# Performance work log

Hardware: AMD Instinct MI355X
Metric: run time of the kernel (lower is better)

## Reference

```python
import jax, jax.numpy as jnp
import numpy as np

B, N, D = 4, 160, 64
ZI, ZE, L, LE = 64, 64, 4, 8
H1, H2 = 128, 64


def setup_inputs() -> dict:
    key = jax.random.key(0)
    ks = jax.random.split(key, 20)
    s = 0.05
    inp = {
        "node_embeddings": jax.random.normal(ks[0], (B, N, D), jnp.float32),
        "z_intra_t": jax.random.normal(ks[1], (B, ZI), jnp.float32),
        "z_inter_t": jax.random.normal(ks[2], (B, ZE), jnp.float32),
        # lag embedding table
        "lag_emb": jax.random.normal(ks[3], (L, LE), jnp.float32),
        # instantaneous reasoner: (2D+ZI)->128->64->1
        "Wi1": jax.random.normal(ks[4], (2 * D + ZI, H1), jnp.float32) * s,
        "bi1": jnp.zeros((H1,), jnp.float32),
        "Wi2": jax.random.normal(ks[5], (H1, H2), jnp.float32) * s,
        "bi2": jnp.zeros((H2,), jnp.float32),
        "Wi3": jax.random.normal(ks[6], (H2, 1), jnp.float32) * s,
        "bi3": jnp.zeros((1,), jnp.float32),
        # lagged reasoner: (2D+ZE+LE)->128->64->1
        "Wl1": jax.random.normal(ks[7], (2 * D + ZE + LE, H1), jnp.float32) * s,
        "bl1": jnp.zeros((H1,), jnp.float32),
        "Wl2": jax.random.normal(ks[8], (H1, H2), jnp.float32) * s,
        "bl2": jnp.zeros((H2,), jnp.float32),
        "Wl3": jax.random.normal(ks[9], (H2, 1), jnp.float32) * s,
        "bl3": jnp.zeros((1,), jnp.float32),
    }
    return inp


def reference(node_embeddings, z_intra_t, z_inter_t, lag_emb,
              Wi1, bi1, Wi2, bi2, Wi3, bi3,
              Wl1, bl1, Wl2, bl2, Wl3, bl3):
    # Instead of materializing concat([h_i, h_j, z, ...]) over N*N pairs,
    # split the first linear layer's weight along its input rows; the sum of
    # per-part projections equals the linear over the concatenation.
    ne = node_embeddings  # [B, N, D]

    # --- instantaneous reasoner ---
    Wi1_a, Wi1_b, Wi1_z = Wi1[:D], Wi1[D:2 * D], Wi1[2 * D:]
    pi = ne @ Wi1_a          # [B, N, H1] projection of h_i
    pj = ne @ Wi1_b          # [B, N, H1] projection of h_j
    pz = z_intra_t @ Wi1_z   # [B, H1]
    h = jax.nn.relu(pi[:, :, None, :] + pj[:, None, :, :]
                    + pz[:, None, None, :] + bi1)          # [B, N, N, H1]
    h = jax.nn.relu(h @ Wi2 + bi2)                         # [B, N, N, H2]
    W_logits = (h @ Wi3 + bi3)[..., 0]                     # [B, N, N]

    # --- lagged reasoner ---
    Wl1_a, Wl1_b = Wl1[:D], Wl1[D:2 * D]
    Wl1_z, Wl1_l = Wl1[2 * D:2 * D + ZE], Wl1[2 * D + ZE:]
    qi = ne @ Wl1_a          # [B, N, H1]
    qj = ne @ Wl1_b          # [B, N, H1]
    qz = z_inter_t @ Wl1_z   # [B, H1]
    ql = lag_emb @ Wl1_l     # [L, H1]
    g = jax.nn.relu(qi[:, None, :, None, :] + qj[:, None, None, :, :]
                    + qz[:, None, None, None, :] + ql[None, :, None, None, :]
                    + bl1)                                 # [B, L, N, N, H1]
    g = jax.nn.relu(g @ Wl2 + bl2)                         # [B, L, N, N, H2]
    A_logits = (g @ Wl3 + bl3)[..., 0]                     # [B, L, N, N]

    mask = 1.0 - jnp.eye(N, dtype=ne.dtype)
    W_t = jax.nn.sigmoid(W_logits) * mask
    A_lags_t = jax.nn.sigmoid(A_logits) * mask
    return (W_t, A_lags_t)
```

## Files before the change

### kernel.cpp

```cpp
#include <hip/hip_runtime.h>
#include <hip/hip_bf16.h>

#define B_   4
#define N_   160
#define D_   64
#define ZI_  64
#define H1_  128
#define H2_  64
#define L_   4
#define LE_  8

typedef __bf16 bf16x8 __attribute__((ext_vector_type(8)));
typedef float  f32x4  __attribute__((ext_vector_type(4)));

__global__ __launch_bounds__(128) void stage_a(
    const float* __restrict__ ne,
    const float* __restrict__ zi,
    const float* __restrict__ ze,
    const float* __restrict__ lag,
    const float* __restrict__ Wi1,
    const float* __restrict__ bi1,
    const float* __restrict__ Wl1,
    const float* __restrict__ bl1,
    const float* __restrict__ Wi2,
    const float* __restrict__ Wl2,
    float* __restrict__ ui, float* __restrict__ uq,
    __bf16* __restrict__ vpi, __bf16* __restrict__ vpl,
    __bf16* __restrict__ W2fi, __bf16* __restrict__ W2fl)
{
    const int bi = blockIdx.x;
    const int b  = bi / N_;
    const int h  = threadIdx.x;

    const float* nerow = ne + bi * D_;

    float pi_ = 0.f, pj_ = 0.f, qi_ = 0.f, qj_ = 0.f;
#pragma unroll 16
    for (int d = 0; d < D_; ++d) {
        const float a = nerow[d];
        pi_ += a * Wi1[d * H1_ + h];
        pj_ += a * Wi1[(D_ + d) * H1_ + h];
        qi_ += a * Wl1[d * H1_ + h];
        qj_ += a * Wl1[(D_ + d) * H1_ + h];
    }
    float pz = 0.f, qz = 0.f;
#pragma unroll 16
    for (int z = 0; z < ZI_; ++z) {
        pz += zi[b * ZI_ + z] * Wi1[(2 * D_ + z) * H1_ + h];
        qz += ze[b * ZI_ + z] * Wl1[(2 * D_ + z) * H1_ + h];
    }

    ui[bi * H1_ + h]  = pi_ + pz + bi1[h];
    vpi[bi * H1_ + h] = (__bf16)pj_;
    vpl[bi * H1_ + h] = (__bf16)qj_;

    const float qbase = qi_ + qz + bl1[h];
#pragma unroll
    for (int l = 0; l < L_; ++l) {
        float ql = 0.f;
#pragma unroll
        for (int e = 0; e < LE_; ++e)
            ql += lag[l * LE_ + e] * Wl1[(2 * D_ + ZI_ + e) * H1_ + h];
        uq[((b * L_ + l) * N_ + (bi % N_)) * H1_ + h] = qbase + ql;
    }

    if (bi < 2) {
        const float* Wsrc = (bi == 0) ? Wi2 : Wl2;
        __bf16* Wdst = (bi == 0) ? W2fi : W2fl;
#pragma unroll
        for (int r = 0; r < 8; ++r) {
            const int fc = h + 128 * r;
            const int kt = fc >> 8, ct = (fc >> 6) & 3;
            const int q = (fc >> 4) & 3, c = fc & 15;
            bf16x8 t;
#pragma unroll
            for (int j = 0; j < 8; ++j)
                t[j] = (__bf16)Wsrc[(32 * kt + 8 * q + j) * H2_ + 16 * ct + c];
            *(bf16x8*)(Wdst + fc * 8) = t;
        }
    }
}

__global__ __launch_bounds__(256, 2) void stage_b(
    const float* __restrict__ ui, const float* __restrict__ uq,
    const __bf16* __restrict__ vpi, const __bf16* __restrict__ vpl,
    const __bf16* __restrict__ W2fi, const __bf16* __restrict__ W2fl,
    const float* __restrict__ bi2, const float* __restrict__ bi3,
    const float* __restrict__ bl2, const float* __restrict__ bl3,
    const float* __restrict__ Wi3, const float* __restrict__ Wl3,
    float* __restrict__ out)
{
    __shared__ __bf16 panel[N_ * H1_];

    const int t    = threadIdx.x;
    const int wid  = t >> 6;
    const int lane = t & 63;
    const int q = lane >> 4;
    const int c = lane & 15;

    const int blk  = blockIdx.x;
    const int wave = blk * 4 + wid;

    const __bf16 *psrc, *Wf;
    if (blk < 160) { psrc = vpi + (blk / 40) * (N_ * H1_);          Wf = W2fi; }
    else           { psrc = vpl + ((blk - 160) / 160) * (N_ * H1_); Wf = W2fl; }

    const float* ubase;
    const float *b2, *w3;
    float b3f;
    long  obase;
    int   i;
    if (wave < B_ * N_) {
        i = wave % N_;
        ubase = ui + wave * H1_;
        b2 = bi2; w3 = Wi3; b3f = bi3[0];
        obase = (long)wave * N_;
    } else {
        const int w2i = wave - B_ * N_;
        i = w2i % N_;
        ubase = uq + w2i * H1_;
        b2 = bl2; w3 = Wl3; b3f = bl3[0];
        obase = (long)B_ * N_ * N_ + (long)w2i * N_;
    }

    bf16x8 stg[10];
#pragma unroll
    for (int it = 0; it < 10; ++it)
        stg[it] = *(const bf16x8*)(psrc + 2048 * it + 8 * t);

    bf16x8 bfr[4][4];
#pragma unroll
    for (int kt = 0; kt < 4; ++kt)
#pragma unroll
        for (int ct = 0; ct < 4; ++ct)
            bfr[kt][ct] = *(const bf16x8*)(Wf + ((kt * 4 + ct) * 64 + lane) * 8);

    f32x4 u0[4], u1[4];
#pragma unroll
    for (int kt = 0; kt < 4; ++kt) {
        const float* up = ubase + 32 * kt + 8 * q;
        u0[kt] = *(const f32x4*)(up);
        u1[kt] = *(const f32x4*)(up + 4);
    }

    float b2c[4], w3c[4];
#pragma unroll
    for (int ct = 0; ct < 4; ++ct) {
        b2c[ct] = b2[16 * ct + c];
        w3c[ct] = w3[16 * ct + c];
    }

    {
        const int gsw = (t & 15) ^ ((t >> 4) & 7);
        const int rowbase = (t >> 4) * H1_ + gsw * 8;
#pragma unroll
        for (int it = 0; it < 10; ++it)
            *(bf16x8*)(panel + 16 * it * H1_ + rowbase) = stg[it];
    }
    __syncthreads();

    for (int jt = 0; jt < 10; ++jt) {
        const __bf16* prow = panel + (16 * jt + c) * H1_;
        f32x4 acc[4];
#pragma unroll
        for (int ct = 0; ct < 4; ++ct)
            acc[ct] = (f32x4){b2c[ct], b2c[ct], b2c[ct], b2c[ct]};

#pragma unroll
        for (int kt = 0; kt < 4; ++kt) {
            const bf16x8 vb = *(const bf16x8*)(prow + (((4 * kt + q) ^ (c & 7)) << 3));
            bf16x8 a;
#pragma unroll
            for (int j = 0; j < 4; ++j) {
                a[j]     = (__bf16)fmaxf(u0[kt][j] + (float)vb[j],     0.f);
                a[4 + j] = (__bf16)fmaxf(u1[kt][j] + (float)vb[4 + j], 0.f);
            }
#pragma unroll
            for (int ct = 0; ct < 4; ++ct)
                acc[ct] = __builtin_amdgcn_mfma_f32_16x16x32_bf16(
                    a, bfr[kt][ct], acc[ct], 0, 0, 0);
        }

        float logit[4];
#pragma unroll
        for (int r = 0; r < 4; ++r) {
            float p = 0.f;
#pragma unroll
            for (int ct = 0; ct < 4; ++ct) {
                const float h2 = fmaxf(acc[ct][r], 0.f);
                p += h2 * w3c[ct];
            }
            p += __shfl_xor(p, 1);
            p += __shfl_xor(p, 2);
            p += __shfl_xor(p, 4);
            p += __shfl_xor(p, 8);
            logit[r] = p;
        }

        if (c < 4) {
            const int j = 16 * jt + 4 * q + c;
            const float lg = logit[c] + b3f;
            const float s = (j == i) ? 0.f : 1.f / (1.f + __expf(-lg));
            out[obase + j] = s;
        }
    }
}

extern "C" void kernel_launch(void* const* d_in, const int* in_sizes, int n_in,
                              void* d_out, int out_size, void* d_ws, size_t ws_size,
                              hipStream_t stream) {
    const float* ne  = (const float*)d_in[0];
    const float* zi  = (const float*)d_in[1];
    const float* ze  = (const float*)d_in[2];
    const float* lag = (const float*)d_in[3];
    const float* Wi1 = (const float*)d_in[4];
    const float* bi1 = (const float*)d_in[5];
    const float* Wi2 = (const float*)d_in[6];
    const float* bi2 = (const float*)d_in[7];
    const float* Wi3 = (const float*)d_in[8];
    const float* bi3 = (const float*)d_in[9];
    const float* Wl1 = (const float*)d_in[10];
    const float* bl1 = (const float*)d_in[11];
    const float* Wl2 = (const float*)d_in[12];
    const float* bl2 = (const float*)d_in[13];
    const float* Wl3 = (const float*)d_in[14];
    const float* bl3 = (const float*)d_in[15];

    float*  ws   = (float*)d_ws;
    float*  ui   = ws;
    float*  uqw  = ws + 81920;
    __bf16* vpi  = (__bf16*)(ws + 409600);
    __bf16* vpl  = vpi + 81920;
    __bf16* W2fi = (__bf16*)(ws + 491520);
    __bf16* W2fl = W2fi + 8192;

    stage_a<<<B_ * N_, 128, 0, stream>>>(ne, zi, ze, lag, Wi1, bi1, Wl1, bl1,
                                         Wi2, Wl2, ui, uqw, vpi, vpl, W2fi, W2fl);

    stage_b<<<(B_ * N_ + B_ * L_ * N_) / 4, 256, 0, stream>>>(
        ui, uqw, vpi, vpl, W2fi, W2fl,
        bi2, bi3, bl2, bl3, Wi3, Wl3,
        (float*)d_out);
}
```

Before: 113.8 us.

## Split stage_b column range across two blocks and batch logit reductions

Each stage_b block now handles half of the j columns (80 rows of the panel), doubling the grid to 1600 blocks and halving LDS per block. This is meant to raise parallelism and occupancy and shorten each block's critical path. The jt loop is also fully unrolled, with the cross-lane shuffle reductions and sigmoid stores deferred until after all MFMA work so they can be batched. In exchange, u/W2 fragment loads and the block prologue are duplicated across twice as many blocks, and register pressure rises.

```diff
diff --git a/kernel.cpp b/kernel.cpp
--- a/kernel.cpp
+++ b/kernel.cpp
@@ -90,7 +90,7 @@
     const float* __restrict__ Wi3, const float* __restrict__ Wl3,
     float* __restrict__ out)
 {
-    __shared__ __bf16 panel[N_ * H1_];
+    __shared__ __bf16 panel[80 * H1_];
 
     const int t    = threadIdx.x;
     const int wid  = t >> 6;
@@ -98,34 +98,38 @@
     const int q = lane >> 4;
     const int c = lane & 15;
 
-    const int blk  = blockIdx.x;
-    const int wave = blk * 4 + wid;
+    const int blk    = blockIdx.x;
+    const int rowgrp = blk >> 1;
+    const int half   = blk & 1;
+    const int wave   = rowgrp * 4 + wid;
 
     const __bf16 *psrc, *Wf;
-    if (blk < 160) { psrc = vpi + (blk / 40) * (N_ * H1_);          Wf = W2fi; }
-    else           { psrc = vpl + ((blk - 160) / 160) * (N_ * H1_); Wf = W2fl; }
+    if (rowgrp < 160) { psrc = vpi + (rowgrp / 40) * (N_ * H1_);           Wf = W2fi; }
+    else              { psrc = vpl + ((rowgrp - 160) / 160) * (N_ * H1_);  Wf = W2fl; }
+    psrc += 80 * half * H1_;
 
     const float* ubase;
     const float *b2, *w3;
-    float b3f;
+    const float* b3p;
     long  obase;
     int   i;
     if (wave < B_ * N_) {
         i = wave % N_;
         ubase = ui + wave * H1_;
-        b2 = bi2; w3 = Wi3; b3f = bi3[0];
+        b2 = bi2; w3 = Wi3; b3p = bi3;
         obase = (long)wave * N_;
     } else {
         const int w2i = wave - B_ * N_;
         i = w2i % N_;
         ubase = uq + w2i * H1_;
-        b2 = bl2; w3 = Wl3; b3f = bl3[0];
+        b2 = bl2; w3 = Wl3; b3p = bl3;
         obase = (long)B_ * N_ * N_ + (long)w2i * N_;
     }
-
-    bf16x8 stg[10];
-#pragma unroll
-    for (int it = 0; it < 10; ++it)
+    const float b3f = b3p[0];
+
+    bf16x8 stg[5];
+#pragma unroll
+    for (int it = 0; it < 5; ++it)
         stg[it] = *(const bf16x8*)(psrc + 2048 * it + 8 * t);
 
     bf16x8 bfr[4][4];
@@ -154,13 +158,15 @@
         const int gsw = (t & 15) ^ ((t >> 4) & 7);
         const int rowbase = (t >> 4) * H1_ + gsw * 8;
 #pragma unroll
-        for (int it = 0; it < 10; ++it)
+        for (int it = 0; it < 5; ++it)
             *(bf16x8*)(panel + 16 * it * H1_ + rowbase) = stg[it];
     }
     __syncthreads();
 
-    for (int jt = 0; jt < 10; ++jt) {
-        const __bf16* prow = panel + (16 * jt + c) * H1_;
+    float plog[5][4];
+#pragma unroll
+    for (int jtl = 0; jtl < 5; ++jtl) {
+        const __bf16* prow = panel + (16 * jtl + c) * H1_;
         f32x4 acc[4];
 #pragma unroll
         for (int ct = 0; ct < 4; ++ct)
@@ -181,25 +187,37 @@
                     a, bfr[kt][ct], acc[ct], 0, 0, 0);
         }
 
-        float logit[4];
 #pragma unroll
         for (int r = 0; r < 4; ++r) {
             float p = 0.f;
 #pragma unroll
-            for (int ct = 0; ct < 4; ++ct) {
-                const float h2 = fmaxf(acc[ct][r], 0.f);
-                p += h2 * w3c[ct];
-            }
+            for (int ct = 0; ct < 4; ++ct)
+                p += fmaxf(acc[ct][r], 0.f) * w3c[ct];
+            plog[jtl][r] = p;
+        }
+    }
+
+#pragma unroll
+    for (int jtl = 0; jtl < 5; ++jtl)
+#pragma unroll
+        for (int r = 0; r < 4; ++r) {
+            float p = plog[jtl][r];
             p += __shfl_xor(p, 1);
             p += __shfl_xor(p, 2);
             p += __shfl_xor(p, 4);
             p += __shfl_xor(p, 8);
-            logit[r] = p;
-        }
-
-        if (c < 4) {
-            const int j = 16 * jt + 4 * q + c;
-            const float lg = logit[c] + b3f;
+            plog[jtl][r] = p;
+        }
+
+    if (c < 4) {
+#pragma unroll
+        for (int jtl = 0; jtl < 5; ++jtl) {
+            float lg = plog[jtl][0];
+            lg = (c == 1) ? plog[jtl][1] : lg;
+            lg = (c == 2) ? plog[jtl][2] : lg;
+            lg = (c == 3) ? plog[jtl][3] : lg;
+            lg += b3f;
+            const int j = 80 * half + 16 * jtl + 4 * q + c;
             const float s = (j == i) ? 0.f : 1.f / (1.f + __expf(-lg));
             out[obase + j] = s;
         }
@@ -237,7 +255,7 @@
     stage_a<<<B_ * N_, 128, 0, stream>>>(ne, zi, ze, lag, Wi1, bi1, Wl1, bl1,
                                          Wi2, Wl2, ui, uqw, vpi, vpl, W2fi, W2fl);
 
-    stage_b<<<(B_ * N_ + B_ * L_ * N_) / 4, 256, 0, stream>>>(
+    stage_b<<<2 * (B_ * N_ + B_ * L_ * N_) / 4, 256, 0, stream>>>(
         ui, uqw, vpi, vpl, W2fi, W2fl,
         bi2, bi3, bl2, bl3, Wi3, Wl3,
         (float*)d_out);
```

Measured after the change: 117.7 us. +3.4%, slower.

## Load panel directly to LDS, pre-swizzle in stage_a, packed bf16 activation math

Applied to the files above, without the earlier changes.

Stage_a now writes the bf16 j-projection rows in the XOR-swizzled layout that stage_b reads. That lets stage_b copy the panel straight from global into LDS with global_load_lds and drop the register staging buffer. The inner loop unpacks bf16 pairs with shifts and masks, runs add and ReLU as vector ops on even/odd lanes, and repacks with a paired bf16 convert. The launch bound occupancy hint goes from 2 to 4 blocks, trading register budget for occupancy, though the 40 KB LDS panel per block may still cap residency.

```diff
diff --git a/kernel.cpp b/kernel.cpp
--- a/kernel.cpp
+++ b/kernel.cpp
@@ -12,6 +12,14 @@
 
 typedef __bf16 bf16x8 __attribute__((ext_vector_type(8)));
 typedef float  f32x4  __attribute__((ext_vector_type(4)));
+typedef unsigned int u32x4 __attribute__((ext_vector_type(4)));
+
+static __device__ __forceinline__ unsigned pk_bf16(float a, float b) {
+    __hip_bfloat162 h = __float22bfloat162_rn(float2{a, b});
+    union { __hip_bfloat162 h; unsigned u; } c;
+    c.h = h;
+    return c.u;
+}
 
 __global__ __launch_bounds__(128) void stage_a(
     const float* __restrict__ ne,
@@ -50,9 +58,11 @@
         qz += ze[b * ZI_ + z] * Wl1[(2 * D_ + z) * H1_ + h];
     }
 
-    ui[bi * H1_ + h]  = pi_ + pz + bi1[h];
-    vpi[bi * H1_ + h] = (__bf16)pj_;
-    vpl[bi * H1_ + h] = (__bf16)qj_;
+    ui[bi * H1_ + h] = pi_ + pz + bi1[h];
+
+    const int hsw = (((h >> 3) ^ (bi & 7)) << 3) | (h & 7);
+    vpi[bi * H1_ + hsw] = (__bf16)pj_;
+    vpl[bi * H1_ + hsw] = (__bf16)qj_;
 
     const float qbase = qi_ + qz + bl1[h];
 #pragma unroll
@@ -81,7 +91,7 @@
     }
 }
 
-__global__ __launch_bounds__(256, 2) void stage_b(
+__global__ __launch_bounds__(256, 4) void stage_b(
     const float* __restrict__ ui, const float* __restrict__ uq,
     const __bf16* __restrict__ vpi, const __bf16* __restrict__ vpl,
     const __bf16* __restrict__ W2fi, const __bf16* __restrict__ W2fl,
@@ -90,7 +100,7 @@
     const float* __restrict__ Wi3, const float* __restrict__ Wl3,
     float* __restrict__ out)
 {
-    __shared__ __bf16 panel[N_ * H1_];
+    __shared__ __align__(16) __bf16 panel[N_ * H1_];
 
     const int t    = threadIdx.x;
     const int wid  = t >> 6;
@@ -105,28 +115,36 @@
     if (blk < 160) { psrc = vpi + (blk / 40) * (N_ * H1_);          Wf = W2fi; }
     else           { psrc = vpl + ((blk - 160) / 160) * (N_ * H1_); Wf = W2fl; }
 
+    {
+        const char* gp = (const char*)psrc;
+        char* lp = (char*)panel;
+#pragma unroll
+        for (int it = 0; it < 10; ++it) {
+            __builtin_amdgcn_global_load_lds(
+                (const __attribute__((address_space(1))) void*)(gp + it * 4096 + t * 16),
+                (__attribute__((address_space(3))) void*)(lp + it * 4096 + wid * 1024),
+                16, 0, 0);
+        }
+    }
+
     const float* ubase;
     const float *b2, *w3;
-    float b3f;
+    const float* b3p;
     long  obase;
     int   i;
     if (wave < B_ * N_) {
         i = wave % N_;
         ubase = ui + wave * H1_;
-        b2 = bi2; w3 = Wi3; b3f = bi3[0];
+        b2 = bi2; w3 = Wi3; b3p = bi3;
         obase = (long)wave * N_;
     } else {
         const int w2i = wave - B_ * N_;
         i = w2i % N_;
         ubase = uq + w2i * H1_;
-        b2 = bl2; w3 = Wl3; b3f = bl3[0];
+        b2 = bl2; w3 = Wl3; b3p = bl3;
         obase = (long)B_ * N_ * N_ + (long)w2i * N_;
     }
-
-    bf16x8 stg[10];
-#pragma unroll
-    for (int it = 0; it < 10; ++it)
-        stg[it] = *(const bf16x8*)(psrc + 2048 * it + 8 * t);
+    const float b3f = b3p[0];
 
     bf16x8 bfr[4][4];
 #pragma unroll
@@ -135,12 +153,13 @@
         for (int ct = 0; ct < 4; ++ct)
             bfr[kt][ct] = *(const bf16x8*)(Wf + ((kt * 4 + ct) * 64 + lane) * 8);
 
-    f32x4 u0[4], u1[4];
+    f32x4 ue[4], uo[4];
 #pragma unroll
     for (int kt = 0; kt < 4; ++kt) {
-        const float* up = ubase + 32 * kt + 8 * q;
-        u0[kt] = *(const f32x4*)(up);
-        u1[kt] = *(const f32x4*)(up + 4);
+        const f32x4 a0 = *(const f32x4*)(ubase + 32 * kt + 8 * q);
+        const f32x4 a1 = *(const f32x4*)(ubase + 32 * kt + 8 * q + 4);
+        ue[kt] = (f32x4){a0[0], a0[2], a1[0], a1[2]};
+        uo[kt] = (f32x4){a0[1], a0[3], a1[1], a1[3]};
     }
 
     float b2c[4], w3c[4];
@@ -150,13 +169,6 @@
         w3c[ct] = w3[16 * ct + c];
     }
 
-    {
-        const int gsw = (t & 15) ^ ((t >> 4) & 7);
-        const int rowbase = (t >> 4) * H1_ + gsw * 8;
-#pragma unroll
-        for (int it = 0; it < 10; ++it)
-            *(bf16x8*)(panel + 16 * it * H1_ + rowbase) = stg[it];
-    }
     __syncthreads();
 
     for (int jt = 0; jt < 10; ++jt) {
@@ -168,17 +180,27 @@
 
 #pragma unroll
         for (int kt = 0; kt < 4; ++kt) {
-            const bf16x8 vb = *(const bf16x8*)(prow + (((4 * kt + q) ^ (c & 7)) << 3));
-            bf16x8 a;
-#pragma unroll
-            for (int j = 0; j < 4; ++j) {
-                a[j]     = (__bf16)fmaxf(u0[kt][j] + (float)vb[j],     0.f);
-                a[4 + j] = (__bf16)fmaxf(u1[kt][j] + (float)vb[4 + j], 0.f);
+            const u32x4 vw = *(const u32x4*)(prow + (((4 * kt + q) ^ (c & 7)) << 3));
+            f32x4 vlo, vhi;
+#pragma unroll
+            for (int d = 0; d < 4; ++d) {
+                const unsigned lo = vw[d] << 16;
+                const unsigned hi = vw[d] & 0xffff0000u;
+                vlo[d] = __uint_as_float(lo);
+                vhi[d] = __uint_as_float(hi);
             }
+            f32x4 xe = ue[kt] + vlo;
+            f32x4 xo = uo[kt] + vhi;
+            xe = __builtin_elementwise_max(xe, (f32x4)0.f);
+            xo = __builtin_elementwise_max(xo, (f32x4)0.f);
+            union { bf16x8 v; unsigned d[4]; } a;
+#pragma unroll
+            for (int d = 0; d < 4; ++d)
+                a.d[d] = pk_bf16(xe[d], xo[d]);
 #pragma unroll
             for (int ct = 0; ct < 4; ++ct)
                 acc[ct] = __builtin_amdgcn_mfma_f32_16x16x32_bf16(
-                    a, bfr[kt][ct], acc[ct], 0, 0, 0);
+                    a.v, bfr[kt][ct], acc[ct], 0, 0, 0);
         }
 
         float logit[4];
@@ -186,10 +208,8 @@
         for (int r = 0; r < 4; ++r) {
             float p = 0.f;
 #pragma unroll
-            for (int ct = 0; ct < 4; ++ct) {
-                const float h2 = fmaxf(acc[ct][r], 0.f);
-                p += h2 * w3c[ct];
-            }
+            for (int ct = 0; ct < 4; ++ct)
+                p += fmaxf(acc[ct][r], 0.f) * w3c[ct];
             p += __shfl_xor(p, 1);
             p += __shfl_xor(p, 2);
             p += __shfl_xor(p, 4);
```

New measurement: 147.6 us. +29.7%, slower.
